# Kernel optimization log

Hardware: AMD Instinct MI355X
Metric: run time of the kernel (lower is better)

The kernel has to match this reference:

```python
import jax, jax.numpy as jnp
import numpy as np

N, D = 8192, 256


def leaky_relu(x):
    return jnp.where(x >= 0, x, 0.1 * x)


def trans_prob(head, dependent, A, b1, b2):
    # x[i,j] = head[i] @ A @ dependent[j] + head[i]@b1 + dependent[j]@b2
    x = (head @ A) @ dependent.T + (head @ b1)[:, None] + (dependent @ b2)[None, :]
    return jax.nn.softmax(x, axis=1)


def soft_gnn(head, dependent, alpha, awh, awd, cwh, cwd):
    # Vectorized form of the nested loop (j != i excluded via diagonal correction):
    # head_agg[i] = sum_j alpha[j,i]*head[j] + alpha[i,j]*dependent[j]  (j != i)
    # dep_agg[i]  = sum_j alpha[i,j]*head[j] + alpha[j,i]*dependent[j]  (j != i)
    d_alpha = jnp.diagonal(alpha)[:, None]  # [n,1]
    hd = head + dependent
    head_agg = alpha.T @ head + alpha @ dependent - d_alpha * hd
    dep_agg = alpha @ head + alpha.T @ dependent - d_alpha * hd
    new_head = leaky_relu(head_agg @ awh + head @ cwh)
    new_dep = leaky_relu(dep_agg @ awd + dependent @ cwd)
    return new_head, new_dep


def setup_inputs() -> dict:
    key = jax.random.key(0)
    ks = jax.random.split(key, 16)
    u = lambda k, shp: jax.random.uniform(k, shp, dtype=jnp.float32)
    return {
        "head": jax.random.normal(ks[0], (N, D), dtype=jnp.float32),
        "dependent": jax.random.normal(ks[1], (N, D), dtype=jnp.float32),
        "tp1_A": u(ks[2], (D, D)), "tp1_b1": u(ks[3], (D,)), "tp1_b2": u(ks[4], (D,)),
        "tp2_A": u(ks[5], (D, D)), "tp2_b1": u(ks[6], (D,)), "tp2_b2": u(ks[7], (D,)),
        "g1_awh": u(ks[8], (D, D)), "g1_awd": u(ks[9], (D, D)),
        "g1_cwh": u(ks[10], (D, D)), "g1_cwd": u(ks[11], (D, D)),
        "g2_awh": u(ks[12], (D, D)), "g2_awd": u(ks[13], (D, D)),
        "g2_cwh": u(ks[14], (D, D)), "g2_cwd": u(ks[15], (D, D)),
    }


def reference(head, dependent, tp1_A, tp1_b1, tp1_b2, tp2_A, tp2_b1, tp2_b2,
              g1_awh, g1_awd, g1_cwh, g1_cwd, g2_awh, g2_awd, g2_cwh, g2_cwd):
    alpha1 = trans_prob(head, dependent, tp1_A, tp1_b1, tp1_b2)
    head, dependent = soft_gnn(head, dependent, alpha1, g1_awh, g1_awd, g1_cwh, g1_cwd)
    alpha2 = trans_prob(head, dependent, tp2_A, tp2_b1, tp2_b2)
    head, dependent = soft_gnn(head, dependent, alpha2, g2_awh, g2_awd, g2_cwh, g2_cwd)
    return head, dependent, alpha1, alpha2
```

## Files before the change

### kernel.cpp

```cpp
#include <hip/hip_runtime.h>

constexpr int N = 8192;
constexpr int D = 256;

typedef __attribute__((ext_vector_type(8))) short short8v;
typedef __attribute__((ext_vector_type(4))) short short4v;
typedef __attribute__((ext_vector_type(4))) float f32x4;

__device__ __forceinline__ const float4* f4c(const float* p) { return reinterpret_cast<const float4*>(p); }
__device__ __forceinline__ float4* f4(float* p) { return reinterpret_cast<float4*>(p); }

__device__ __forceinline__ short f2bf(float f) {
    unsigned u = __builtin_bit_cast(unsigned, f);
    u += 0x7fff + ((u >> 16) & 1);
    return (short)(u >> 16);
}
__device__ __forceinline__ float bf2f(short s) {
    unsigned u = ((unsigned)(unsigned short)s) << 16;
    return __builtin_bit_cast(float, u);
}
template <int NS>
__device__ __forceinline__ void splitN(float x, short* s) {
    s[0] = f2bf(x);
    if constexpr (NS > 1) {
        float r = x - bf2f(s[0]);
        s[1] = f2bf(r);
        s[2] = f2bf(r - bf2f(s[1]));
    }
}

__global__ __launch_bounds__(512) void spmm_scan8(const float* __restrict__ M0,
                                                  const float* __restrict__ M1,
                                                  const float* __restrict__ H,
                                                  const float* __restrict__ Dp,
                                                  float* __restrict__ S,
                                                  float* __restrict__ T) {
    const float* __restrict__ M = blockIdx.y ? M1 : M0;
    float* __restrict__ out = blockIdx.y ? T : S;
    const int row = blockIdx.x;
    const int w = threadIdx.x >> 6;
    const int lane = threadIdx.x & 63;
    const float* __restrict__ src = (lane < 32) ? H : Dp;
    const int c0 = (lane & 31) * 8;

    const float4* rp = f4c(M + (size_t)row * N) + w * 256;
    float4 v[4];
#pragma unroll
    for (int q = 0; q < 4; q++) v[q] = rp[q * 64 + lane];

    float4 acc0 = {0.f, 0.f, 0.f, 0.f}, acc1 = {0.f, 0.f, 0.f, 0.f};
#pragma unroll
    for (int q = 0; q < 4; q++) {
        float va[4] = {v[q].x, v[q].y, v[q].z, v[q].w};
#pragma unroll
        for (int e = 0; e < 4; e++) {
            unsigned long long mask = __ballot(va[e] != 0.0f);
            while (mask) {
                int l = __builtin_ctzll(mask);
                mask &= mask - 1;
                float a = __shfl(va[e], l);
                int j = w * 1024 + q * 256 + l * 4 + e;
                const float* xr = src + (size_t)j * D + c0;
                float4 x0 = *f4c(xr);
                float4 x1 = *f4c(xr + 4);
                acc0.x = fmaf(a, x0.x, acc0.x);
                acc0.y = fmaf(a, x0.y, acc0.y);
                acc0.z = fmaf(a, x0.z, acc0.z);
                acc0.w = fmaf(a, x0.w, acc0.w);
                acc1.x = fmaf(a, x1.x, acc1.x);
                acc1.y = fmaf(a, x1.y, acc1.y);
                acc1.z = fmaf(a, x1.z, acc1.z);
                acc1.w = fmaf(a, x1.w, acc1.w);
            }
        }
    }

    __shared__ float part[8][512];
    const int colbase = c0 + ((lane < 32) ? 0 : 256);
    *f4(&part[w][colbase]) = acc0;
    *f4(&part[w][colbase + 4]) = acc1;
    __syncthreads();
    const int t = threadIdx.x;
    float s = 0.f;
#pragma unroll
    for (int ww = 0; ww < 8; ww++) s += part[ww][t];
    out[(size_t)row * 512 + t] = s;
}

__global__ __launch_bounds__(256) void transpose_kernel(const float* __restrict__ in,
                                                        float* __restrict__ outT) {
    __shared__ float tile[64][65];
    const int t = threadIdx.x;
    const int i0 = blockIdx.y * 64;
    const int j0 = blockIdx.x * 64;
    const int r = t >> 2;
    const int c0 = (t & 3) * 16;
#pragma unroll
    for (int q = 0; q < 4; q++) {
        float4 v = *f4c(in + (size_t)(i0 + r) * N + j0 + c0 + q * 4);
        tile[r][c0 + q * 4 + 0] = v.x;
        tile[r][c0 + q * 4 + 1] = v.y;
        tile[r][c0 + q * 4 + 2] = v.z;
        tile[r][c0 + q * 4 + 3] = v.w;
    }
    __syncthreads();
#pragma unroll
    for (int q = 0; q < 4; q++) {
        float4 o = {tile[c0 + q * 4 + 0][r], tile[c0 + q * 4 + 1][r],
                    tile[c0 + q * 4 + 2][r], tile[c0 + q * 4 + 3][r]};
        *f4(outT + (size_t)(j0 + r) * N + i0 + c0 + q * 4) = o;
    }
}

template <int NTERMS, int TRANS>
__global__ __launch_bounds__(256, NTERMS == 1 ? 3 : 2)
void agg_mfma(const float* __restrict__ alpha, const float* __restrict__ H,
              const float* __restrict__ Dp, float* __restrict__ out) {
    constexpr int NS = (NTERMS == 1) ? 1 : 3;
    __shared__ short As[NS][128][40];
    __shared__ short Bs[NS][128][40];
    const int t = threadIdx.x;
    const int bx = blockIdx.x;
    const int i0 = blockIdx.y * 128;
    const float* Bsrc = (bx < 2) ? (H + bx * 128) : (Dp + (bx - 2) * 128);
    const int lane = t & 63;
    const int w = t >> 6;
    const int wm = w >> 1, wn = w & 1;
    const int fr = lane & 15, fq = lane >> 4;
    f32x4 acc[4][4];
#pragma unroll
    for (int a = 0; a < 4; a++)
#pragma unroll
        for (int b = 0; b < 4; b++) acc[a][b] = (f32x4){0.f, 0.f, 0.f, 0.f};
    const int sm = t >> 1;
    const int skh = (t & 1) << 4;
    const int skk = t >> 3;
    const int sc0 = (t & 7) << 4;
#pragma unroll 1
    for (int k0 = 0; k0 < N; k0 += 32) {
        if constexpr (TRANS == 0) {
            const float* src = alpha + (size_t)(i0 + sm) * N + k0 + skh;
            const int swz = (sm >> 4) & 3;
#pragma unroll
            for (int q = 0; q < 4; q++) {
                float4 v = f4c(src)[q];
                int k = skh + 4 * q;
                int col = ((((k >> 3) ^ swz)) << 3) | (k & 4);
                float vv[4] = {v.x, v.y, v.z, v.w};
                short a0[4], a1[4], a2[4];
#pragma unroll
                for (int e = 0; e < 4; e++) {
                    short tmp[3];
                    splitN<NS>(vv[e], tmp);
                    a0[e] = tmp[0]; a1[e] = tmp[1]; a2[e] = tmp[2];
                }
                *(short4v*)&As[0][sm][col] = (short4v){a0[0], a0[1], a0[2], a0[3]};
                if constexpr (NTERMS > 1) {
                    *(short4v*)&As[1][sm][col] = (short4v){a1[0], a1[1], a1[2], a1[3]};
                    *(short4v*)&As[2][sm][col] = (short4v){a2[0], a2[1], a2[2], a2[3]};
                }
            }
        } else {
            const float* src = alpha + (size_t)(k0 + skk) * N + i0 + sc0;
#pragma unroll
            for (int q = 0; q < 4; q++) {
                float4 v = f4c(src)[q];
                float vv[4] = {v.x, v.y, v.z, v.w};
#pragma unroll
                for (int e = 0; e < 4; e++) {
                    int m = sc0 + 4 * q + e;
                    int swz = (m >> 4) & 3;
                    int col = (skk & 7) | ((((skk >> 3) ^ swz)) << 3);
                    short tmp[3];
                    splitN<NS>(vv[e], tmp);
                    As[0][m][col] = tmp[0];
                    if constexpr (NTERMS > 1) { As[1][m][col] = tmp[1]; As[2][m][col] = tmp[2]; }
                }
            }
        }
        {
            const float* src = Bsrc + (size_t)(k0 + skk) * D + sc0;
#pragma unroll
            for (int q = 0; q < 4; q++) {
                float4 v = f4c(src)[q];
                float vv[4] = {v.x, v.y, v.z, v.w};
#pragma unroll
                for (int e = 0; e < 4; e++) {
                    int n = sc0 + 4 * q + e;
                    int swz = (n >> 4) & 3;
                    int col = (skk & 7) | ((((skk >> 3) ^ swz)) << 3);
                    short tmp[3];
                    splitN<NS>(vv[e], tmp);
                    Bs[0][n][col] = tmp[0];
                    if constexpr (NTERMS > 1) { Bs[1][n][col] = tmp[1]; Bs[2][n][col] = tmp[2]; }
                }
            }
        }
        __syncthreads();
        short8v af[NS][4], bg[NS][4];
#pragma unroll
        for (int mr = 0; mr < 4; mr++) {
            int row = wm * 64 + mr * 16 + fr;
            int cidx = 8 * (fq ^ ((wm * 4 + mr) & 3));
#pragma unroll
            for (int s = 0; s < NS; s++) af[s][mr] = *(const short8v*)&As[s][row][cidx];
        }
#pragma unroll
        for (int nr = 0; nr < 4; nr++) {
            int rowb = wn * 64 + nr * 16 + fr;
            int cidx = 8 * (fq ^ ((wn * 4 + nr) & 3));
#pragma unroll
            for (int s = 0; s < NS; s++) bg[s][nr] = *(const short8v*)&Bs[s][rowb][cidx];
        }
#pragma unroll
        for (int mr = 0; mr < 4; mr++) {
#pragma unroll
            for (int nr = 0; nr < 4; nr++) {
                f32x4 a = acc[mr][nr];
                a = __builtin_amdgcn_mfma_f32_16x16x32_bf16(af[0][mr], bg[0][nr], a, 0, 0, 0);
                if constexpr (NTERMS > 1) {
                    a = __builtin_amdgcn_mfma_f32_16x16x32_bf16(af[0][mr], bg[1][nr], a, 0, 0, 0);
                    a = __builtin_amdgcn_mfma_f32_16x16x32_bf16(af[1][mr], bg[0][nr], a, 0, 0, 0);
                    a = __builtin_amdgcn_mfma_f32_16x16x32_bf16(af[1][mr], bg[1][nr], a, 0, 0, 0);
                    a = __builtin_amdgcn_mfma_f32_16x16x32_bf16(af[0][mr], bg[2][nr], a, 0, 0, 0);
                    a = __builtin_amdgcn_mfma_f32_16x16x32_bf16(af[2][mr], bg[0][nr], a, 0, 0, 0);
                }
                acc[mr][nr] = a;
            }
        }
        __syncthreads();
    }
#pragma unroll
    for (int mr = 0; mr < 4; mr++) {
#pragma unroll
        for (int nr = 0; nr < 4; nr++) {
            int col = bx * 128 + wn * 64 + nr * 16 + fr;
#pragma unroll
            for (int j = 0; j < 4; j++) {
                int row = i0 + wm * 64 + mr * 16 + fq * 4 + j;
                out[(size_t)row * 512 + col] = acc[mr][nr][j];
            }
        }
    }
}

__global__ __launch_bounds__(256) void rowdot_kernel(const float* __restrict__ X,
                                                     const float* __restrict__ v,
                                                     float* __restrict__ out) {
    int lane = threadIdx.x & 63;
    int row = blockIdx.x * 4 + (threadIdx.x >> 6);
    float4 a = f4c(X + (size_t)row * D)[lane];
    float4 b = f4c(v)[lane];
    float s = a.x * b.x + a.y * b.y + a.z * b.z + a.w * b.w;
#pragma unroll
    for (int off = 32; off > 0; off >>= 1) s += __shfl_down(s, off);
    if (lane == 0) out[row] = s;
}

__global__ __launch_bounds__(256) void gemm_nk256_kernel(const float* __restrict__ A,
                                                         const float* __restrict__ W,
                                                         float* __restrict__ C) {
    __shared__ float As[16][68];
    __shared__ float Bs[16][68];
    int t = threadIdx.x;
    int tx = t & 15, ty = t >> 4;
    int j0 = blockIdx.x * 64;
    int i0 = blockIdx.y * 64;
    float acc[4][4] = {};
    for (int k0 = 0; k0 < 256; k0 += 16) {
        {
            int m = t >> 2, k4 = (t & 3) * 4;
            float4 a = *f4c(A + (size_t)(i0 + m) * D + k0 + k4);
            As[k4 + 0][m] = a.x; As[k4 + 1][m] = a.y; As[k4 + 2][m] = a.z; As[k4 + 3][m] = a.w;
            int kk = t >> 4, c = (t & 15) * 4;
            *f4(&Bs[kk][c]) = *f4c(W + (size_t)(k0 + kk) * D + j0 + c);
        }
        __syncthreads();
#pragma unroll
        for (int kk = 0; kk < 16; kk++) {
            float4 av = *f4c(&As[kk][ty * 4]);
            float4 bv = *f4c(&Bs[kk][tx * 4]);
            float a[4] = {av.x, av.y, av.z, av.w};
            float b[4] = {bv.x, bv.y, bv.z, bv.w};
#pragma unroll
            for (int r = 0; r < 4; r++)
#pragma unroll
                for (int c = 0; c < 4; c++) acc[r][c] = fmaf(a[r], b[c], acc[r][c]);
        }
        __syncthreads();
    }
#pragma unroll
    for (int r = 0; r < 4; r++) {
        float4 o = {acc[r][0], acc[r][1], acc[r][2], acc[r][3]};
        *f4(C + (size_t)(i0 + ty * 4 + r) * D + j0 + tx * 4) = o;
    }
}

__global__ __launch_bounds__(256) void update_kernel(const float* __restrict__ A1,
                                                     const float* __restrict__ W1,
                                                     const float* __restrict__ A2,
                                                     const float* __restrict__ W2,
                                                     float* __restrict__ C) {
    __shared__ float As[16][68];
    __shared__ float Bs[16][68];
    int t = threadIdx.x;
    int tx = t & 15, ty = t >> 4;
    int j0 = blockIdx.x * 64;
    int i0 = blockIdx.y * 64;
    float acc[4][4] = {};
#pragma unroll 1
    for (int pass = 0; pass < 2; pass++) {
        const float* Ap = pass ? A2 : A1;
        const float* Wp = pass ? W2 : W1;
        for (int k0 = 0; k0 < 256; k0 += 16) {
            {
                int m = t >> 2, k4 = (t & 3) * 4;
                float4 a = *f4c(Ap + (size_t)(i0 + m) * D + k0 + k4);
                As[k4 + 0][m] = a.x; As[k4 + 1][m] = a.y; As[k4 + 2][m] = a.z; As[k4 + 3][m] = a.w;
                int kk = t >> 4, c = (t & 15) * 4;
                *f4(&Bs[kk][c]) = *f4c(Wp + (size_t)(k0 + kk) * D + j0 + c);
            }
            __syncthreads();
#pragma unroll
            for (int kk = 0; kk < 16; kk++) {
                float4 av = *f4c(&As[kk][ty * 4]);
                float4 bv = *f4c(&Bs[kk][tx * 4]);
                float a[4] = {av.x, av.y, av.z, av.w};
                float b[4] = {bv.x, bv.y, bv.z, bv.w};
#pragma unroll
                for (int r = 0; r < 4; r++)
#pragma unroll
                    for (int c = 0; c < 4; c++) acc[r][c] = fmaf(a[r], b[c], acc[r][c]);
            }
            __syncthreads();
        }
    }
#pragma unroll
    for (int r = 0; r < 4; r++) {
        float o[4];
#pragma unroll
        for (int c = 0; c < 4; c++) {
            float x = acc[r][c];
            o[c] = x >= 0.f ? x : 0.1f * x;
        }
        float4 ov = {o[0], o[1], o[2], o[3]};
        *f4(C + (size_t)(i0 + ty * 4 + r) * D + j0 + tx * 4) = ov;
    }
}

__global__ __launch_bounds__(256) void logits_kernel(const float* __restrict__ Z,
                                                     const float* __restrict__ Dp,
                                                     const float* __restrict__ bh,
                                                     const float* __restrict__ bd,
                                                     float* __restrict__ alpha) {
    __shared__ float As[32][132];
    __shared__ float Bs[32][132];
    int t = threadIdx.x;
    int tx = t & 15, ty = t >> 4;
    int j0 = blockIdx.x * 128;
    int i0 = blockIdx.y * 128;
    float acc[8][8] = {};
    for (int k0 = 0; k0 < 256; k0 += 32) {
#pragma unroll
        for (int r = 0; r < 4; r++) {
            int fid = r * 256 + t;
            int m = fid >> 3, k4 = (fid & 7) * 4;
            float4 a = *f4c(Z + (size_t)(i0 + m) * D + k0 + k4);
            As[k4 + 0][m] = a.x; As[k4 + 1][m] = a.y; As[k4 + 2][m] = a.z; As[k4 + 3][m] = a.w;
            float4 b = *f4c(Dp + (size_t)(j0 + m) * D + k0 + k4);
            Bs[k4 + 0][m] = b.x; Bs[k4 + 1][m] = b.y; Bs[k4 + 2][m] = b.z; Bs[k4 + 3][m] = b.w;
        }
        __syncthreads();
#pragma unroll 4
        for (int kk = 0; kk < 32; kk++) {
            float4 a0 = *f4c(&As[kk][ty * 8]);
            float4 a1 = *f4c(&As[kk][ty * 8 + 4]);
            float4 b0 = *f4c(&Bs[kk][tx * 8]);
            float4 b1 = *f4c(&Bs[kk][tx * 8 + 4]);
            float a[8] = {a0.x, a0.y, a0.z, a0.w, a1.x, a1.y, a1.z, a1.w};
            float b[8] = {b0.x, b0.y, b0.z, b0.w, b1.x, b1.y, b1.z, b1.w};
#pragma unroll
            for (int r = 0; r < 8; r++)
#pragma unroll
                for (int c = 0; c < 8; c++) acc[r][c] = fmaf(a[r], b[c], acc[r][c]);
        }
        __syncthreads();
    }
    float4 bd0 = *f4c(bd + j0 + tx * 8);
    float4 bd1 = *f4c(bd + j0 + tx * 8 + 4);
#pragma unroll
    for (int r = 0; r < 8; r++) {
        float bhr = bh[i0 + ty * 8 + r];
        float4 o0 = {acc[r][0] + bhr + bd0.x, acc[r][1] + bhr + bd0.y,
                     acc[r][2] + bhr + bd0.z, acc[r][3] + bhr + bd0.w};
        float4 o1 = {acc[r][4] + bhr + bd1.x, acc[r][5] + bhr + bd1.y,
                     acc[r][6] + bhr + bd1.z, acc[r][7] + bhr + bd1.w};
        float* orow = alpha + (size_t)(i0 + ty * 8 + r) * N + j0 + tx * 8;
        f4(orow)[0] = o0;
        f4(orow)[1] = o1;
    }
}

__global__ __launch_bounds__(256) void softmax_kernel(float* __restrict__ alpha) {
    int row = blockIdx.x;
    int t = threadIdx.x;
    float4* rp = f4(alpha + (size_t)row * N);
    float4 v[8];
    float m = -3.4e38f;
#pragma unroll
    for (int i = 0; i < 8; i++) {
        v[i] = rp[i * 256 + t];
        m = fmaxf(m, fmaxf(fmaxf(v[i].x, v[i].y), fmaxf(v[i].z, v[i].w)));
    }
    __shared__ float red[8];
#pragma unroll
    for (int off = 32; off > 0; off >>= 1) m = fmaxf(m, __shfl_xor(m, off));
    if ((t & 63) == 0) red[t >> 6] = m;
    __syncthreads();
    m = fmaxf(fmaxf(red[0], red[1]), fmaxf(red[2], red[3]));
    float s = 0.f;
#pragma unroll
    for (int i = 0; i < 8; i++) {
        v[i].x = __expf(v[i].x - m);
        v[i].y = __expf(v[i].y - m);
        v[i].z = __expf(v[i].z - m);
        v[i].w = __expf(v[i].w - m);
        s += v[i].x + v[i].y + v[i].z + v[i].w;
    }
#pragma unroll
    for (int off = 32; off > 0; off >>= 1) s += __shfl_xor(s, off);
    if ((t & 63) == 0) red[4 + (t >> 6)] = s;
    __syncthreads();
    s = red[4] + red[5] + red[6] + red[7];
    float inv = 1.f / s;
#pragma unroll
    for (int i = 0; i < 8; i++) {
        v[i].x *= inv; v[i].y *= inv; v[i].z *= inv; v[i].w *= inv;
        rp[i * 256 + t] = v[i];
    }
}

__global__ __launch_bounds__(256) void diag_kernel(const float* __restrict__ alpha,
                                                   float* __restrict__ da) {
    int i = blockIdx.x * 256 + threadIdx.x;
    da[i] = alpha[(size_t)i * N + i];
}

__global__ __launch_bounds__(256) void combine_kernel(const float* __restrict__ S,
                                                      const float* __restrict__ T,
                                                      const float* __restrict__ da,
                                                      const float* __restrict__ H,
                                                      const float* __restrict__ Dp,
                                                      float* __restrict__ hagg,
                                                      float* __restrict__ dagg) {
    int gid = blockIdx.x * 256 + threadIdx.x;
    int i = gid >> 6;
    int d4 = (gid & 63) * 4;
    float a = da[i];
    float4 sH = *f4c(S + (size_t)i * (2 * D) + d4);
    float4 sD = *f4c(S + (size_t)i * (2 * D) + D + d4);
    float4 tH = *f4c(T + (size_t)i * (2 * D) + d4);
    float4 tD = *f4c(T + (size_t)i * (2 * D) + D + d4);
    float4 h = *f4c(H + (size_t)i * D + d4);
    float4 dp = *f4c(Dp + (size_t)i * D + d4);
    float4 hd = {h.x + dp.x, h.y + dp.y, h.z + dp.z, h.w + dp.w};
    float4 ha = {tH.x + sD.x - a * hd.x, tH.y + sD.y - a * hd.y,
                 tH.z + sD.z - a * hd.z, tH.w + sD.w - a * hd.w};
    float4 dg = {sH.x + tD.x - a * hd.x, sH.y + tD.y - a * hd.y,
                 sH.z + tD.z - a * hd.z, sH.w + tD.w - a * hd.w};
    *f4(hagg + (size_t)i * D + d4) = ha;
    *f4(dagg + (size_t)i * D + d4) = dg;
}

extern "C" void kernel_launch(void* const* d_in, const int* in_sizes, int n_in,
                              void* d_out, int out_size, void* d_ws, size_t ws_size,
                              hipStream_t stream) {
    const float* head = (const float*)d_in[0];
    const float* dep = (const float*)d_in[1];
    const float* tpA[2] = {(const float*)d_in[2], (const float*)d_in[5]};
    const float* tpb1[2] = {(const float*)d_in[3], (const float*)d_in[6]};
    const float* tpb2[2] = {(const float*)d_in[4], (const float*)d_in[7]};
    const float* awh[2] = {(const float*)d_in[8], (const float*)d_in[12]};
    const float* awd[2] = {(const float*)d_in[9], (const float*)d_in[13]};
    const float* cwh[2] = {(const float*)d_in[10], (const float*)d_in[14]};
    const float* cwd[2] = {(const float*)d_in[11], (const float*)d_in[15]};

    float* out = (float*)d_out;
    float* outHead = out;
    float* outDep = out + (size_t)N * D;
    float* alpha1 = out + (size_t)2 * N * D;
    float* alpha2 = alpha1 + (size_t)N * N;

    float* w = (float*)d_ws;
    float* S = w;               w += (size_t)N * 2 * D;
    float* Z = S;
    float* T = w;               w += (size_t)N * 2 * D;
    float* bh = w;              w += N;
    float* bd = w;              w += N;
    float* da = w;              w += N;
    float* hagg = w;            w += (size_t)N * D;
    float* dagg = w;            w += (size_t)N * D;
    float* H1 = w;              w += (size_t)N * D;
    float* D1 = w;              w += (size_t)N * D;
    float* alphaT = w;          w += (size_t)N * N;
    size_t needed = ((char*)w) - (char*)d_ws;
    const bool use_sparse = (ws_size >= needed);

    for (int L = 0; L < 2; L++) {
        const float* Hin = L ? H1 : head;
        const float* Din = L ? D1 : dep;
        float* Hout = L ? outHead : H1;
        float* Dout = L ? outDep : D1;
        float* alpha = L ? alpha2 : alpha1;

        rowdot_kernel<<<N / 4, 256, 0, stream>>>(Hin, tpb1[L], bh);
        rowdot_kernel<<<N / 4, 256, 0, stream>>>(Din, tpb2[L], bd);
        gemm_nk256_kernel<<<dim3(D / 64, N / 64), 256, 0, stream>>>(Hin, tpA[L], Z);
        logits_kernel<<<dim3(N / 128, N / 128), 256, 0, stream>>>(Z, Din, bh, bd, alpha);
        softmax_kernel<<<N, 256, 0, stream>>>(alpha);
        diag_kernel<<<N / 256, 256, 0, stream>>>(alpha, da);
        if (use_sparse) {
            transpose_kernel<<<dim3(N / 64, N / 64), 256, 0, stream>>>(alpha, alphaT);
            spmm_scan8<<<dim3(N, 2), 512, 0, stream>>>(alpha, alphaT, Hin, Din, S, T);
        } else {
            if (L == 0) {
                agg_mfma<6, 0><<<dim3(4, N / 128), 256, 0, stream>>>(alpha, Hin, Din, S);
                agg_mfma<6, 1><<<dim3(4, N / 128), 256, 0, stream>>>(alpha, Hin, Din, T);
            } else {
                agg_mfma<1, 0><<<dim3(4, N / 128), 256, 0, stream>>>(alpha, Hin, Din, S);
                agg_mfma<1, 1><<<dim3(4, N / 128), 256, 0, stream>>>(alpha, Hin, Din, T);
            }
        }
        combine_kernel<<<(N * D / 4) / 256, 256, 0, stream>>>(S, T, da, Hin, Din, hagg, dagg);
        update_kernel<<<dim3(D / 64, N / 64), 256, 0, stream>>>(hagg, awh[L], Hin, cwh[L], Hout);
        update_kernel<<<dim3(D / 64, N / 64), 256, 0, stream>>>(dagg, awd[L], Din, cwd[L], Dout);
    }
}
```

Before: 2.041 ms.

## Compute logits GEMM on bf16 MFMA with multi-limb float splitting

The fp32 logits GEMM (Z times dependent transposed, plus biases) is replaced by a matrix-core kernel. Z and dependent are first split into two or three bf16 limbs by a separate pre-pass. The kernel then accumulates 3 or 6 cross-limb MFMA products to approximate fp32 accuracy: fewer limbs in layer 1, more in layer 2. This is meant to move the large N×N×D product off the vector ALUs. In exchange it adds split passes, extra workspace and some precision risk. The fast path now also needs more workspace, so the sparse aggregation path depends on the larger workspace requirement.

Result: faster. 1.635 ms (-19.9%).

```diff
diff --git a/kernel.cpp b/kernel.cpp
--- a/kernel.cpp
+++ b/kernel.cpp
@@ -26,6 +26,118 @@
         float r = x - bf2f(s[0]);
         s[1] = f2bf(r);
         s[2] = f2bf(r - bf2f(s[1]));
+    }
+}
+
+template <int NL>
+__global__ __launch_bounds__(256) void split_limbs(const float* __restrict__ src,
+                                                   unsigned short* __restrict__ dst) {
+    const size_t ND = (size_t)N * D;
+    int gid = blockIdx.x * 256 + threadIdx.x;
+    float4 v0 = f4c(src)[gid * 2];
+    float4 v1 = f4c(src)[gid * 2 + 1];
+    float vv[8] = {v0.x, v0.y, v0.z, v0.w, v1.x, v1.y, v1.z, v1.w};
+    short sp[3][8];
+#pragma unroll
+    for (int e = 0; e < 8; e++) {
+        short tmp[3];
+        splitN<NL>(vv[e], tmp);
+        sp[0][e] = tmp[0];
+        if constexpr (NL > 1) { sp[1][e] = tmp[1]; sp[2][e] = tmp[2]; }
+    }
+#pragma unroll
+    for (int s = 0; s < NL; s++)
+        *(short8v*)(dst + s * ND + (size_t)gid * 8) =
+            (short8v){sp[s][0], sp[s][1], sp[s][2], sp[s][3],
+                      sp[s][4], sp[s][5], sp[s][6], sp[s][7]};
+}
+
+template <int NL, int NPROD>
+__global__ __launch_bounds__(256, 2)
+void logits_mfma(const unsigned short* __restrict__ zP,
+                 const unsigned short* __restrict__ dP,
+                 const float* __restrict__ bh, const float* __restrict__ bd,
+                 float* __restrict__ alpha) {
+    __shared__ unsigned short As[NL][128][40];
+    __shared__ unsigned short Bs[NL][128][40];
+    const int t = threadIdx.x;
+    const int j0 = blockIdx.x * 128;
+    const int i0 = blockIdx.y * 128;
+    const size_t PS = (size_t)N * D;
+    const int lane = t & 63, w = t >> 6, wm = w >> 1, wn = w & 1;
+    const int fr = lane & 15, fq = lane >> 4;
+
+    f32x4 acc[4][4];
+#pragma unroll
+    for (int a = 0; a < 4; a++)
+#pragma unroll
+        for (int b = 0; b < 4; b++) acc[a][b] = (f32x4){0.f, 0.f, 0.f, 0.f};
+
+#pragma unroll 1
+    for (int k0 = 0; k0 < D; k0 += 32) {
+#pragma unroll
+        for (int s = 0; s < NL; s++) {
+#pragma unroll
+            for (int g = 0; g < 2; g++) {
+                int gid = g * 256 + t;
+                int m = gid >> 2, gk = gid & 3;
+                int col = (gk ^ ((m >> 4) & 3)) << 3;
+                short8v va = *(const short8v*)(zP + s * PS + (size_t)(i0 + m) * D + k0 + gk * 8);
+                *(short8v*)&As[s][m][col] = va;
+                short8v vb = *(const short8v*)(dP + s * PS + (size_t)(j0 + m) * D + k0 + gk * 8);
+                *(short8v*)&Bs[s][m][col] = vb;
+            }
+        }
+        __syncthreads();
+
+        short8v af[NL][4], bg[NL][4];
+#pragma unroll
+        for (int mr = 0; mr < 4; mr++) {
+            int row = wm * 64 + mr * 16 + fr;
+            int cidx = 8 * (fq ^ ((wm * 4 + mr) & 3));
+#pragma unroll
+            for (int s = 0; s < NL; s++) af[s][mr] = *(const short8v*)&As[s][row][cidx];
+        }
+#pragma unroll
+        for (int nr = 0; nr < 4; nr++) {
+            int rowb = wn * 64 + nr * 16 + fr;
+            int cidx = 8 * (fq ^ ((wn * 4 + nr) & 3));
+#pragma unroll
+            for (int s = 0; s < NL; s++) bg[s][nr] = *(const short8v*)&Bs[s][rowb][cidx];
+        }
+#pragma unroll
+        for (int mr = 0; mr < 4; mr++) {
+#pragma unroll
+            for (int nr = 0; nr < 4; nr++) {
+                f32x4 a = acc[mr][nr];
+                a = __builtin_amdgcn_mfma_f32_16x16x32_bf16(af[0][mr], bg[0][nr], a, 0, 0, 0);
+                if constexpr (NPROD >= 3) {
+                    a = __builtin_amdgcn_mfma_f32_16x16x32_bf16(af[0][mr], bg[1][nr], a, 0, 0, 0);
+                    a = __builtin_amdgcn_mfma_f32_16x16x32_bf16(af[1][mr], bg[0][nr], a, 0, 0, 0);
+                }
+                if constexpr (NPROD >= 6) {
+                    a = __builtin_amdgcn_mfma_f32_16x16x32_bf16(af[1][mr], bg[1][nr], a, 0, 0, 0);
+                    a = __builtin_amdgcn_mfma_f32_16x16x32_bf16(af[0][mr], bg[2][nr], a, 0, 0, 0);
+                    a = __builtin_amdgcn_mfma_f32_16x16x32_bf16(af[2][mr], bg[0][nr], a, 0, 0, 0);
+                }
+                acc[mr][nr] = a;
+            }
+        }
+        __syncthreads();
+    }
+
+#pragma unroll
+    for (int nr = 0; nr < 4; nr++) {
+        int col = j0 + wn * 64 + nr * 16 + fr;
+        float bdv = bd[col];
+#pragma unroll
+        for (int mr = 0; mr < 4; mr++) {
+#pragma unroll
+            for (int j = 0; j < 4; j++) {
+                int row = i0 + wm * 64 + mr * 16 + fq * 4 + j;
+                alpha[(size_t)row * N + col] = acc[mr][nr][j] + bh[row] + bdv;
+            }
+        }
     }
 }
 
@@ -503,8 +615,10 @@
     float* H1 = w;              w += (size_t)N * D;
     float* D1 = w;              w += (size_t)N * D;
     float* alphaT = w;          w += (size_t)N * N;
-    size_t needed = ((char*)w) - (char*)d_ws;
-    const bool use_sparse = (ws_size >= needed);
+    unsigned short* zP = (unsigned short*)w;
+    unsigned short* dP = zP + (size_t)3 * N * D;
+    size_t needed = ((char*)(dP + (size_t)3 * N * D)) - (char*)d_ws;
+    const bool use_fast = (ws_size >= needed);
 
     for (int L = 0; L < 2; L++) {
         const float* Hin = L ? H1 : head;
@@ -516,10 +630,22 @@
         rowdot_kernel<<<N / 4, 256, 0, stream>>>(Hin, tpb1[L], bh);
         rowdot_kernel<<<N / 4, 256, 0, stream>>>(Din, tpb2[L], bd);
         gemm_nk256_kernel<<<dim3(D / 64, N / 64), 256, 0, stream>>>(Hin, tpA[L], Z);
-        logits_kernel<<<dim3(N / 128, N / 128), 256, 0, stream>>>(Z, Din, bh, bd, alpha);
+        if (use_fast) {
+            if (L == 0) {
+                split_limbs<2><<<N * D / 8 / 256, 256, 0, stream>>>(Z, zP);
+                split_limbs<2><<<N * D / 8 / 256, 256, 0, stream>>>(Din, dP);
+                logits_mfma<2, 3><<<dim3(N / 128, N / 128), 256, 0, stream>>>(zP, dP, bh, bd, alpha);
+            } else {
+                split_limbs<3><<<N * D / 8 / 256, 256, 0, stream>>>(Z, zP);
+                split_limbs<3><<<N * D / 8 / 256, 256, 0, stream>>>(Din, dP);
+                logits_mfma<3, 6><<<dim3(N / 128, N / 128), 256, 0, stream>>>(zP, dP, bh, bd, alpha);
+            }
+        } else {
+            logits_kernel<<<dim3(N / 128, N / 128), 256, 0, stream>>>(Z, Din, bh, bd, alpha);
+        }
         softmax_kernel<<<N, 256, 0, stream>>>(alpha);
         diag_kernel<<<N / 256, 256, 0, stream>>>(alpha, da);
-        if (use_sparse) {
+        if (use_fast) {
             transpose_kernel<<<dim3(N / 64, N / 64), 256, 0, stream>>>(alpha, alphaT);
             spmm_scan8<<<dim3(N, 2), 512, 0, stream>>>(alpha, alphaT, Hin, Din, S, T);
         } else {
```
